# Kernel optimization log

Hardware: AMD Instinct MI355X
Metric: run time of the kernel (lower is better)

Reference implementation:

```python
import jax, jax.numpy as jnp
import numpy as np

SHAPES = ((80, 80), (40, 40), (20, 20), (10, 10))  # (H, W) per level
N_HEADS = 8
N_POINTS = 4
D_MODEL = 512  # double_d_model = 2*256 (densefusion=True)
D_FFN = 1024
B = 2
L = len(SHAPES)
S = sum(h * w for h, w in SHAPES)  # 8500
EPS = 1e-5


def _layernorm(x, g, b):
    m = jnp.mean(x, axis=-1, keepdims=True)
    v = jnp.mean((x - m) ** 2, axis=-1, keepdims=True)
    return (x - m) * jax.lax.rsqrt(v + EPS) * g + b


def _reference_points(shapes):
    # encoder get_reference_points with valid_ratios == 1 -> [S, 2] (x, y) in (0,1)
    refs = []
    for (H, W) in shapes:
        ry = (jnp.arange(H, dtype=jnp.float32) + 0.5) / H
        rx = (jnp.arange(W, dtype=jnp.float32) + 0.5) / W
        gy, gx = jnp.meshgrid(ry, rx, indexing='ij')
        refs.append(jnp.stack([gx.reshape(-1), gy.reshape(-1)], axis=-1))
    return jnp.concatenate(refs, axis=0)


def _sample_level(val, loc, H, W):
    # val: [B, H*W, h, d]; loc: [B, S, h, P, 2] normalized in [0,1]
    b, _, h, d = val.shape
    s, p = loc.shape[1], loc.shape[3]
    x = loc[..., 0] * W - 0.5
    y = loc[..., 1] * H - 0.5
    x0 = jnp.floor(x)
    y0 = jnp.floor(y)
    wx = x - x0
    wy = y - y0
    x0i = x0.astype(jnp.int32)
    y0i = y0.astype(jnp.int32)

    def gather(xi, yi):
        valid = ((xi >= 0) & (xi < W) & (yi >= 0) & (yi < H)).astype(val.dtype)
        idx = jnp.clip(yi, 0, H - 1) * W + jnp.clip(xi, 0, W - 1)  # [B,S,h,P]
        idx2 = jnp.transpose(idx, (0, 1, 3, 2)).reshape(b, s * p, h)  # [B,S*P,h]
        g = jnp.take_along_axis(val, idx2[..., None], axis=1)  # [B,S*P,h,d]
        vmask = jnp.transpose(valid, (0, 1, 3, 2))[..., None]  # [B,S,P,h,1]
        return g.reshape(b, s, p, h, d) * vmask

    v00 = gather(x0i, y0i)
    v01 = gather(x0i + 1, y0i)
    v10 = gather(x0i, y0i + 1)
    v11 = gather(x0i + 1, y0i + 1)
    wxT = jnp.transpose(wx, (0, 1, 3, 2))[..., None]
    wyT = jnp.transpose(wy, (0, 1, 3, 2))[..., None]
    return (v00 * (1 - wxT) * (1 - wyT) + v01 * wxT * (1 - wyT)
            + v10 * (1 - wxT) * wyT + v11 * wxT * wyT)  # [B,S,P,h,d]


def _forward(src, pos, w_off, b_off, w_attn, b_attn, w_val, b_val, w_out, b_out,
             ln1_g, ln1_b, w1, b1, w2, b2, ln2_g, ln2_b, shapes):
    b, s, c = src.shape
    h, p, l = N_HEADS, N_POINTS, len(shapes)
    d = c // h
    q = src + pos
    value = (src @ w_val + b_val).reshape(b, s, h, d)
    offsets = (q @ w_off + b_off).reshape(b, s, h, l, p, 2)
    attn = jax.nn.softmax((q @ w_attn + b_attn).reshape(b, s, h, l * p), axis=-1)
    attn = attn.reshape(b, s, h, l, p)
    ref = _reference_points(shapes)  # [S,2]
    # offset normalizer = (W_l, H_l)
    norm = jnp.array([[W, H] for (H, W) in shapes], dtype=src.dtype)  # [L,2]
    loc = ref[None, :, None, None, None, :] + offsets / norm[None, None, None, :, None, :]
    # split value per level and sample
    starts = np.cumsum([0] + [H * W for (H, W) in shapes])[:-1]
    sampled = []
    for lvl, (H, W) in enumerate(shapes):
        val_l = jax.lax.dynamic_slice_in_dim(value, int(starts[lvl]), H * W, axis=1)
        sampled.append(_sample_level(val_l, loc[:, :, :, lvl], H, W))
    sampled = jnp.stack(sampled)  # [L,B,S,P,h,d]
    out = jnp.einsum('lbqphd,bqhlp->bqhd', sampled, attn).reshape(b, s, c)
    attn_out = out @ w_out + b_out
    x = _layernorm(src + attn_out, ln1_g, ln1_b)
    ffn = jax.nn.relu(x @ w1 + b1) @ w2 + b2
    return _layernorm(x + ffn, ln2_g, ln2_b)


def setup_inputs() -> dict:
    key = jax.random.key(0)
    ks = jax.random.split(key, 20)
    sc = 0.02
    C = D_MODEL
    hLP = N_HEADS * L * N_POINTS
    f32 = jnp.float32
    inp = {
        'src': jax.random.normal(ks[0], (B, S, C), f32),
        'pos': jax.random.normal(ks[1], (B, S, C), f32),
        'w_off': jax.random.normal(ks[2], (C, hLP * 2), f32) * sc,
        'b_off': jax.random.normal(ks[3], (hLP * 2,), f32) * sc,
        'w_attn': jax.random.normal(ks[4], (C, hLP), f32) * sc,
        'b_attn': jax.random.normal(ks[5], (hLP,), f32) * sc,
        'w_val': jax.random.normal(ks[6], (C, C), f32) * sc,
        'b_val': jnp.zeros((C,), f32),
        'w_out': jax.random.normal(ks[7], (C, C), f32) * sc,
        'b_out': jnp.zeros((C,), f32),
        'ln1_g': jnp.ones((C,), f32),
        'ln1_b': jnp.zeros((C,), f32),
        'w1': jax.random.normal(ks[8], (C, D_FFN), f32) * sc,
        'b1': jnp.zeros((D_FFN,), f32),
        'w2': jax.random.normal(ks[9], (D_FFN, C), f32) * sc,
        'b2': jnp.zeros((C,), f32),
        'ln2_g': jnp.ones((C,), f32),
        'ln2_b': jnp.zeros((C,), f32),
        'spatial_shapes': jnp.array(SHAPES, dtype=jnp.int32),
    }
    return inp


def reference(src, pos, w_off, b_off, w_attn, b_attn, w_val, b_val, w_out, b_out,
              ln1_g, ln1_b, w1, b1, w2, b2, ln2_g, ln2_b, spatial_shapes):
    shapes = tuple((int(a), int(b)) for a, b in np.asarray(spatial_shapes))
    return _forward(src, pos, w_off, b_off, w_attn, b_attn, w_val, b_val, w_out, b_out,
                    ln1_g, ln1_b, w1, b1, w2, b2, ln2_g, ln2_b, shapes)
```

## Files before the change

kernel.cpp:

```cpp
#include <hip/hip_runtime.h>


typedef __bf16 bf16_t;
typedef __bf16 bf16x8 __attribute__((ext_vector_type(8)));
typedef __bf16 bf16x4 __attribute__((ext_vector_type(4)));
typedef float  f32x2  __attribute__((ext_vector_type(2)));
typedef float  f32x4  __attribute__((ext_vector_type(4)));
typedef float  f32x16 __attribute__((ext_vector_type(16)));

#define M_ROWS 17000
#define S_LEN  8500

__device__ inline void store_c(float* p, float v)  { *p = v; }
__device__ inline void store_c(bf16_t* p, float v) { *p = (bf16_t)v; }

__device__ inline float4 load4f(const float* p)  { return *(const float4*)p; }
__device__ inline float4 load4f(const bf16_t* p) {
    bf16x4 v = *(const bf16x4*)p;
    return make_float4((float)v[0], (float)v[1], (float)v[2], (float)v[3]);
}

__device__ inline void pk_fma(f32x2& a, f32x2 x, f32x2 y) {
    asm("v_pk_fma_f32 %0, %1, %2, %0" : "+v"(a) : "v"(x), "v"(y));
}

__device__ inline int swz_flat() {
    int o   = blockIdx.x + gridDim.x * blockIdx.y;
    int nwg = gridDim.x * gridDim.y;
    int q = nwg >> 3, r = nwg & 7;
    int xcd = o & 7, s = o >> 3;
    return (xcd < r ? xcd * (q + 1) : r * (q + 1) + (xcd - r) * q) + s;
}

__global__ __launch_bounds__(256)
void prep_kernel(const float* __restrict__ w_val, const float* __restrict__ w_off,
                 const float* __restrict__ w_attn, const float* __restrict__ w_out,
                 const float* __restrict__ w1, const float* __restrict__ w2,
                 const float* __restrict__ b_off, const float* __restrict__ b_attn,
                 bf16_t* __restrict__ wt_val, bf16_t* __restrict__ wt_oa,
                 bf16_t* __restrict__ wt_out, bf16_t* __restrict__ wt_w1,
                 bf16_t* __restrict__ wt_w2, float* __restrict__ bias_oa) {
    int z = blockIdx.z;
    if (z == 6) {
        if (blockIdx.x == 0 && blockIdx.y == 0) {
            for (int i = threadIdx.x; i < 384; i += 256)
                bias_oa[i] = (i < 256) ? b_off[i] : b_attn[i - 256];
        }
        return;
    }
    const float* in; bf16_t* out; int K, N;
    switch (z) {
        case 0: in = w_val;  out = wt_val;                     K = 512;  N = 512;  break;
        case 1: in = w_off;  out = wt_oa;                      K = 512;  N = 256;  break;
        case 2: in = w_attn; out = wt_oa + (size_t)256 * 512;  K = 512;  N = 128;  break;
        case 3: in = w_out;  out = wt_out;                     K = 512;  N = 512;  break;
        case 4: in = w1;     out = wt_w1;                      K = 512;  N = 1024; break;
        default: in = w2;    out = wt_w2;                      K = 1024; N = 512;  break;
    }
    int k0 = blockIdx.x * 32, n0 = blockIdx.y * 32;
    if (k0 >= K || n0 >= N) return;
    __shared__ float s[32][33];
    int tx = threadIdx.x & 31, ty = threadIdx.x >> 5;
    #pragma unroll
    for (int i = 0; i < 4; i++)
        s[ty + 8 * i][tx] = in[(size_t)(k0 + ty + 8 * i) * N + n0 + tx];
    __syncthreads();
    #pragma unroll
    for (int i = 0; i < 4; i++)
        out[(size_t)(n0 + ty + 8 * i) * K + k0 + tx] = (bf16_t)s[tx][ty + 8 * i];
}

__global__ __launch_bounds__(256)
void add_q_kernel(const float* __restrict__ a, const float* __restrict__ b,
                  bf16_t* __restrict__ q, bf16_t* __restrict__ src_bf, int n4) {
    int i = blockIdx.x * 256 + threadIdx.x;
    if (i >= n4) return;
    float4 av = *(const float4*)(a + (size_t)i * 4);
    float4 bv = *(const float4*)(b + (size_t)i * 4);
    bf16x4 sv, ov;
    sv[0] = (bf16_t)av.x; sv[1] = (bf16_t)av.y; sv[2] = (bf16_t)av.z; sv[3] = (bf16_t)av.w;
    ov[0] = (bf16_t)(av.x + bv.x);
    ov[1] = (bf16_t)(av.y + bv.y);
    ov[2] = (bf16_t)(av.z + bv.z);
    ov[3] = (bf16_t)(av.w + bv.w);
    *(bf16x4*)(q      + (size_t)i * 4) = ov;
    *(bf16x4*)(src_bf + (size_t)i * 4) = sv;
}

#define GEMM_CORE(A_PTR, WT_PTR, K_DIM, EPILOGUE)                                  \
    const int tid  = threadIdx.x;                                                  \
    const int wave = tid >> 6;                                                     \
    const int lane = tid & 63;                                                     \
    const int l31  = lane & 31;                                                    \
    const int lh8  = (lane >> 5) * 8;                                              \
    const int wr   = (wave >> 1) * 64;                                             \
    const int wc   = (wave & 1) * 64;                                              \
    const int sr = tid >> 2;                                                       \
    const int sc = (tid & 3) * 8;                                                  \
    const bf16_t* gA0 = A_PTR  + (size_t)min(row0 + sr,      M_ROWS - 1) * (K_DIM) + sc; \
    const bf16_t* gA1 = A_PTR  + (size_t)min(row0 + sr + 64, M_ROWS - 1) * (K_DIM) + sc; \
    const bf16_t* gB0 = WT_PTR + (size_t)(col0 + sr) * (K_DIM) + sc;               \
    const bf16_t* gB1 = WT_PTR + (size_t)(col0 + sr + 64) * (K_DIM) + sc;          \
    f32x16 acc[2][2];                                                              \
    _Pragma("unroll")                                                              \
    for (int i = 0; i < 2; i++)                                                    \
        _Pragma("unroll")                                                          \
        for (int j = 0; j < 2; j++)                                                \
            _Pragma("unroll")                                                      \
            for (int r = 0; r < 16; r++) acc[i][j][r] = 0.f;                       \
    bf16x8 pa0 = *(const bf16x8*)gA0;                                              \
    bf16x8 pa1 = *(const bf16x8*)gA1;                                              \
    bf16x8 pb0 = *(const bf16x8*)gB0;                                              \
    bf16x8 pb1 = *(const bf16x8*)gB1;                                              \
    const int nIter = (K_DIM) >> 5;                                                \
    for (int it = 0; it < nIter; it++) {                                           \
        const int cur = it & 1;                                                    \
        *(bf16x8*)&As[cur][sr][sc]      = pa0;                                     \
        *(bf16x8*)&As[cur][sr + 64][sc] = pa1;                                     \
        *(bf16x8*)&Bs[cur][sr][sc]      = pb0;                                     \
        *(bf16x8*)&Bs[cur][sr + 64][sc] = pb1;                                     \
        __syncthreads();                                                           \
        if (it + 1 < nIter) {                                                      \
            int ko = (it + 1) << 5;                                                \
            pa0 = *(const bf16x8*)(gA0 + ko);                                      \
            pa1 = *(const bf16x8*)(gA1 + ko);                                      \
            pb0 = *(const bf16x8*)(gB0 + ko);                                      \
            pb1 = *(const bf16x8*)(gB1 + ko);                                      \
        }                                                                          \
        _Pragma("unroll")                                                          \
        for (int kh = 0; kh < 2; kh++) {                                           \
            bf16x8 a0 = *(const bf16x8*)&As[cur][wr + l31     ][kh * 16 + lh8];    \
            bf16x8 a1 = *(const bf16x8*)&As[cur][wr + 32 + l31][kh * 16 + lh8];    \
            bf16x8 b0 = *(const bf16x8*)&Bs[cur][wc + l31     ][kh * 16 + lh8];    \
            bf16x8 b1 = *(const bf16x8*)&Bs[cur][wc + 32 + l31][kh * 16 + lh8];    \
            acc[0][0] = __builtin_amdgcn_mfma_f32_32x32x16_bf16(a0, b0, acc[0][0], 0, 0, 0); \
            acc[0][1] = __builtin_amdgcn_mfma_f32_32x32x16_bf16(a0, b1, acc[0][1], 0, 0, 0); \
            acc[1][0] = __builtin_amdgcn_mfma_f32_32x32x16_bf16(a1, b0, acc[1][0], 0, 0, 0); \
            acc[1][1] = __builtin_amdgcn_mfma_f32_32x32x16_bf16(a1, b1, acc[1][1], 0, 0, 0); \
        }                                                                          \
    }                                                                              \
    EPILOGUE

#define GEMM64_CORE(A_PTR, WT_PTR, K_DIM, EPILOGUE)                                \
    const int tid  = threadIdx.x;                                                  \
    const int wave = tid >> 6;                                                     \
    const int lane = tid & 63;                                                     \
    const int l31  = lane & 31;                                                    \
    const int lh8  = (lane >> 5) * 8;                                              \
    const int wr   = wave * 32;                                                    \
    const int sr = tid >> 2;                                                       \
    const int sc = (tid & 3) * 8;                                                  \
    const bf16_t* gA0 = A_PTR  + (size_t)min(row0 + sr,      M_ROWS - 1) * (K_DIM) + sc; \
    const bf16_t* gA1 = A_PTR  + (size_t)min(row0 + sr + 64, M_ROWS - 1) * (K_DIM) + sc; \
    const bf16_t* gB0 = WT_PTR + (size_t)(col0 + sr) * (K_DIM) + sc;               \
    f32x16 acc[2];                                                                 \
    _Pragma("unroll")                                                              \
    for (int j = 0; j < 2; j++)                                                    \
        _Pragma("unroll")                                                          \
        for (int r = 0; r < 16; r++) acc[j][r] = 0.f;                              \
    bf16x8 pa0 = *(const bf16x8*)gA0;                                              \
    bf16x8 pa1 = *(const bf16x8*)gA1;                                              \
    bf16x8 pb0 = *(const bf16x8*)gB0;                                              \
    const int nIter = (K_DIM) >> 5;                                                \
    for (int it = 0; it < nIter; it++) {                                           \
        const int cur = it & 1;                                                    \
        *(bf16x8*)&As[cur][sr][sc]      = pa0;                                     \
        *(bf16x8*)&As[cur][sr + 64][sc] = pa1;                                     \
        *(bf16x8*)&Bs[cur][sr][sc]      = pb0;                                     \
        __syncthreads();                                                           \
        if (it + 1 < nIter) {                                                      \
            int ko = (it + 1) << 5;                                                \
            pa0 = *(const bf16x8*)(gA0 + ko);                                      \
            pa1 = *(const bf16x8*)(gA1 + ko);                                      \
            pb0 = *(const bf16x8*)(gB0 + ko);                                      \
        }                                                                          \
        _Pragma("unroll")                                                          \
        for (int kh = 0; kh < 2; kh++) {                                           \
            bf16x8 a0 = *(const bf16x8*)&As[cur][wr + l31][kh * 16 + lh8];         \
            bf16x8 b0 = *(const bf16x8*)&Bs[cur][l31     ][kh * 16 + lh8];         \
            bf16x8 b1 = *(const bf16x8*)&Bs[cur][32 + l31][kh * 16 + lh8];         \
            acc[0] = __builtin_amdgcn_mfma_f32_32x32x16_bf16(a0, b0, acc[0], 0, 0, 0); \
            acc[1] = __builtin_amdgcn_mfma_f32_32x32x16_bf16(a0, b1, acc[1], 0, 0, 0); \
        }                                                                          \
    }                                                                              \
    EPILOGUE

template<typename OT, bool RELU, int KD>
__global__ __launch_bounds__(256)
void gemm128_kernel(const bf16_t* __restrict__ A, const bf16_t* __restrict__ Wt,
                    const float* __restrict__ bias, OT* __restrict__ Cout, int N) {
    __shared__ bf16_t As[2][128][40];
    __shared__ bf16_t Bs[2][128][40];
    const int wg = swz_flat();
    const int NY = gridDim.y;
    const int row0 = (wg / NY) * 128;
    const int col0 = (wg % NY) * 128;
    GEMM_CORE(A, Wt, KD,
        {
            _Pragma("unroll")
            for (int i = 0; i < 2; i++)
                _Pragma("unroll")
                for (int j = 0; j < 2; j++) {
                    int col = col0 + wc + j * 32 + l31;
                    float bcol = bias[col];
                    _Pragma("unroll")
                    for (int reg = 0; reg < 16; reg++) {
                        int row = row0 + wr + i * 32 + (reg & 3) + 8 * (reg >> 2) + 4 * (lane >> 5);
                        if (row < M_ROWS) {
                            float v = acc[i][j][reg] + bcol;
                            if (RELU) v = fmaxf(v, 0.f);
                            store_c(Cout + (size_t)row * N + col, v);
                        }
                    }
                }
        }
    )
}

template<typename OT, bool RELU, int KD>
__global__ __launch_bounds__(256)
void gemm64_kernel(const bf16_t* __restrict__ A, const bf16_t* __restrict__ Wt,
                   const float* __restrict__ bias, OT* __restrict__ Cout, int N) {
    __shared__ bf16_t As[2][128][40];
    __shared__ bf16_t Bs[2][64][40];
    const int wg = swz_flat();
    const int NY = gridDim.y;
    const int row0 = (wg / NY) * 128;
    const int col0 = (wg % NY) * 64;
    GEMM64_CORE(A, Wt, KD,
        {
            _Pragma("unroll")
            for (int j = 0; j < 2; j++) {
                int col = col0 + j * 32 + l31;
                float bcol = bias[col];
                _Pragma("unroll")
                for (int reg = 0; reg < 16; reg++) {
                    int row = row0 + wr + (reg & 3) + 8 * (reg >> 2) + 4 * (lane >> 5);
                    if (row < M_ROWS) {
                        float v = acc[j][reg] + bcol;
                        if (RELU) v = fmaxf(v, 0.f);
                        store_c(Cout + (size_t)row * N + col, v);
                    }
                }
            }
        }
    )
}

__global__ __launch_bounds__(256)
void gemm_voa_kernel(const bf16_t* __restrict__ src_bf, const bf16_t* __restrict__ q,
                     const bf16_t* __restrict__ wt_val, const bf16_t* __restrict__ wt_oa,
                     const float* __restrict__ b_val, const float* __restrict__ bias_oa,
                     bf16_t* __restrict__ value, float* __restrict__ oa) {
    __shared__ bf16_t As[2][128][40];
    __shared__ bf16_t Bs[2][64][40];
    const int wg = swz_flat();
    const int by = wg % 14;
    const bool isV  = by < 8;
    const int col0  = (isV ? by : by - 8) * 64;
    const int row0  = (wg / 14) * 128;
    const bf16_t* Ap  = isV ? src_bf : q;
    const bf16_t* Wp  = isV ? wt_val : wt_oa;
    const float* bp   = isV ? b_val : bias_oa;
    GEMM64_CORE(Ap, Wp, 512,
        {
            _Pragma("unroll")
            for (int j = 0; j < 2; j++) {
                int col = col0 + j * 32 + l31;
                float bcol = bp[col];
                _Pragma("unroll")
                for (int reg = 0; reg < 16; reg++) {
                    int row = row0 + wr + (reg & 3) + 8 * (reg >> 2) + 4 * (lane >> 5);
                    if (row < M_ROWS) {
                        float v = acc[j][reg] + bcol;
                        if (isV) value[(size_t)row * 512 + col] = (bf16_t)v;
                        else     oa[(size_t)row * 384 + col] = v;
                    }
                }
            }
        }
    )
}

__global__ __launch_bounds__(256)
void sample_kernel(const bf16_t* __restrict__ value, const float* __restrict__ oa,
                   bf16_t* __restrict__ out) {
    __shared__ __align__(16) int sAW[4][2][8][68];
    const int wave = threadIdx.x >> 6;
    const int lane = threadIdx.x & 63;
    const int h    = lane >> 3;
    const int sub  = lane & 7;
    const int bs   = swz_flat() * 4 + wave;
    const int b    = bs / S_LEN;
    const int s    = bs - b * S_LEN;

    float rx, ry;
    if (s < 6400)      { int i = s;        const float inv = 1.f/80.f; ry = ((i/80) + 0.5f)*inv; rx = ((i%80) + 0.5f)*inv; }
    else if (s < 8000) { int i = s - 6400; const float inv = 1.f/40.f; ry = ((i/40) + 0.5f)*inv; rx = ((i%40) + 0.5f)*inv; }
    else if (s < 8400) { int i = s - 8000; const float inv = 1.f/20.f; ry = ((i/20) + 0.5f)*inv; rx = ((i%20) + 0.5f)*inv; }
    else               { int i = s - 8400; const float inv = 1.f/10.f; ry = ((i/10) + 0.5f)*inv; rx = ((i%10) + 0.5f)*inv; }

    const int WH[4]  = {80, 40, 20, 10};
    const int LST[4] = {0, 6400, 8000, 8400};
    const int ll = sub >> 1;
    const int W  = WH[ll];
    const int LS = LST[ll];

    const float* row = oa + (size_t)bs * 384;
    float4 o4 = *(const float4*)(row + h * 32 + sub * 4);
    float2 lg = *(const float2*)(row + 256 + h * 16 + sub * 2);

    float mx = fmaxf(lg.x, lg.y);
    mx = fmaxf(mx, __shfl_xor(mx, 1, 64));
    mx = fmaxf(mx, __shfl_xor(mx, 2, 64));
    mx = fmaxf(mx, __shfl_xor(mx, 4, 64));
    float e0 = __expf(lg.x - mx), e1 = __expf(lg.y - mx);
    float sm = e0 + e1;
    sm += __shfl_xor(sm, 1, 64);
    sm += __shfl_xor(sm, 2, 64);
    sm += __shfl_xor(sm, 4, 64);
    float pinv = 1.f / sm;

    #pragma unroll
    for (int t = 0; t < 2; t++) {
        float ox = t ? o4.z : o4.x;
        float oy = t ? o4.w : o4.y;
        float p  = (t ? e1 : e0) * pinv;
        float x = fmaf(rx, (float)W, ox) - 0.5f;
        float y = fmaf(ry, (float)W, oy) - 0.5f;
        float fx = floorf(x), fy = floorf(y);
        float wx = x - fx, wy = y - fy;
        int ix = (int)fx, iy = (int)fy;
        #pragma unroll
        for (int k2 = 0; k2 < 4; k2++) {
            int cx = ix + (k2 & 1);
            int cy = iy + (k2 >> 1);
            float wgt = p * ((k2 & 1) ? wx : 1.f - wx) * ((k2 >> 1) ? wy : 1.f - wy);
            if (cx < 0 || cx >= W || cy < 0 || cy >= W) wgt = 0.f;
            int xc = min(max(cx, 0), W - 1);
            int yc = min(max(cy, 0), W - 1);
            int c = sub * 8 + t * 4 + k2;
            sAW[wave][0][h][c] = LS + yc * W + xc;
            sAW[wave][1][h][c] = __float_as_int(wgt);
        }
    }
    __syncthreads();

    const bf16_t* vb = value + ((size_t)b * S_LEN) * 512 + h * 64 + sub * 8;
    f32x2 a01 = {0.f, 0.f}, a23 = {0.f, 0.f}, a45 = {0.f, 0.f}, a67 = {0.f, 0.f};

    #define ACC8(V, WW) {                                                          \
        f32x2 ws; ws[0] = (WW); ws[1] = (WW);                                      \
        f32x2 pv;                                                                  \
        pv[0] = __uint_as_float((V).x << 16);                                      \
        pv[1] = __uint_as_float((V).x & 0xffff0000u); pk_fma(a01, pv, ws);         \
        pv[0] = __uint_as_float((V).y << 16);                                      \
        pv[1] = __uint_as_float((V).y & 0xffff0000u); pk_fma(a23, pv, ws);         \
        pv[0] = __uint_as_float((V).z << 16);                                      \
        pv[1] = __uint_as_float((V).z & 0xffff0000u); pk_fma(a45, pv, ws);         \
        pv[0] = __uint_as_float((V).w << 16);                                      \
        pv[1] = __uint_as_float((V).w & 0xffff0000u); pk_fma(a67, pv, ws); }

    #pragma unroll 2
    for (int c8 = 0; c8 < 64; c8 += 8) {
        int4   ia = *(const int4*)  &sAW[wave][0][h][c8];
        int4   ib = *(const int4*)  &sAW[wave][0][h][c8 + 4];
        float4 wa = *(const float4*)&sAW[wave][1][h][c8];
        float4 wb = *(const float4*)&sAW[wave][1][h][c8 + 4];
        uint4 v0 = *(const uint4*)(vb + (size_t)ia.x * 512);
        uint4 v1 = *(const uint4*)(vb + (size_t)ia.y * 512);
        uint4 v2 = *(const uint4*)(vb + (size_t)ia.z * 512);
        uint4 v3 = *(const uint4*)(vb + (size_t)ia.w * 512);
        uint4 v4 = *(const uint4*)(vb + (size_t)ib.x * 512);
        uint4 v5 = *(const uint4*)(vb + (size_t)ib.y * 512);
        uint4 v6 = *(const uint4*)(vb + (size_t)ib.z * 512);
        uint4 v7 = *(const uint4*)(vb + (size_t)ib.w * 512);
        ACC8(v0, wa.x) ACC8(v1, wa.y) ACC8(v2, wa.z) ACC8(v3, wa.w)
        ACC8(v4, wb.x) ACC8(v5, wb.y) ACC8(v6, wb.z) ACC8(v7, wb.w)
    }
    #undef ACC8

    bf16x8 ov;
    ov[0] = (bf16_t)a01[0]; ov[1] = (bf16_t)a01[1];
    ov[2] = (bf16_t)a23[0]; ov[3] = (bf16_t)a23[1];
    ov[4] = (bf16_t)a45[0]; ov[5] = (bf16_t)a45[1];
    ov[6] = (bf16_t)a67[0]; ov[7] = (bf16_t)a67[1];
    *(bf16x8*)(out + (size_t)bs * 512 + h * 64 + sub * 8) = ov;
}

template<typename INA, typename INB, typename OT>
__global__ __launch_bounds__(256)
void ln_kernel(const INA* __restrict__ Xa, const INB* __restrict__ Xb,
               const float* __restrict__ g, const float* __restrict__ be,
               OT* __restrict__ out, int M) {
    int wave = threadIdx.x >> 6;
    int lane = threadIdx.x & 63;
    int row = blockIdx.x * 4 + wave;
    if (row >= M) return;
    size_t base = (size_t)row * 512;
    float v[8];
    float s = 0.f, sq = 0.f;
    #pragma unroll
    for (int p = 0; p < 2; p++) {
        int idx = p * 256 + lane * 4;
        float4 a4 = load4f(Xa + base + idx);
        float4 b4 = load4f(Xb + base + idx);
        float t0 = a4.x + b4.x, t1 = a4.y + b4.y, t2 = a4.z + b4.z, t3 = a4.w + b4.w;
        v[p*4+0] = t0; v[p*4+1] = t1; v[p*4+2] = t2; v[p*4+3] = t3;
        s  += t0 + t1 + t2 + t3;
        sq += t0*t0 + t1*t1 + t2*t2 + t3*t3;
    }
    #pragma unroll
    for (int off = 32; off > 0; off >>= 1) {
        s  += __shfl_xor(s, off, 64);
        sq += __shfl_xor(sq, off, 64);
    }
    float mean = s * (1.f / 512.f);
    float var  = sq * (1.f / 512.f) - mean * mean;
    float rstd = rsqrtf(var + 1e-5f);
    #pragma unroll
    for (int p = 0; p < 2; p++) {
        int idx = p * 256 + lane * 4;
        #pragma unroll
        for (int j = 0; j < 4; j++) {
            int col = idx + j;
            float o = (v[p*4+j] - mean) * rstd * g[col] + be[col];
            store_c(out + base + col, o);
        }
    }
}

extern "C" void kernel_launch(void* const* d_in, const int* in_sizes, int n_in,
                              void* d_out, int out_size, void* d_ws, size_t ws_size,
                              hipStream_t stream) {
    const float* src    = (const float*)d_in[0];
    const float* pos    = (const float*)d_in[1];
    const float* w_off  = (const float*)d_in[2];
    const float* b_off  = (const float*)d_in[3];
    const float* w_attn = (const float*)d_in[4];
    const float* b_attn = (const float*)d_in[5];
    const float* w_val  = (const float*)d_in[6];
    const float* b_val  = (const float*)d_in[7];
    const float* w_out  = (const float*)d_in[8];
    const float* b_out  = (const float*)d_in[9];
    const float* ln1_g  = (const float*)d_in[10];
    const float* ln1_b  = (const float*)d_in[11];
    const float* w1     = (const float*)d_in[12];
    const float* b1     = (const float*)d_in[13];
    const float* w2     = (const float*)d_in[14];
    const float* b2     = (const float*)d_in[15];
    const float* ln2_g  = (const float*)d_in[16];
    const float* ln2_b  = (const float*)d_in[17];

    const int M = M_ROWS;
    char* ws = (char*)d_ws;
    size_t o = 0;
    auto alloc = [&](size_t bytes) { size_t r = o; o += (bytes + 255) & ~(size_t)255; return r; };

    size_t off_q       = alloc((size_t)M * 512 * 2);
    size_t off_srcbf   = alloc((size_t)M * 512 * 2);
    size_t off_value   = alloc((size_t)M * 512 * 2);
    size_t off_sampled = alloc((size_t)M * 512 * 2);
    size_t off_oa      = alloc((size_t)M * 384 * 4);
    size_t off_attnout = alloc((size_t)M * 512 * 2);
    size_t off_x       = alloc((size_t)M * 512 * 2);
    size_t off_wtval   = alloc((size_t)512 * 512 * 2);
    size_t off_wtoa    = alloc((size_t)384 * 512 * 2);
    size_t off_wtout   = alloc((size_t)512 * 512 * 2);
    size_t off_wtw1    = alloc((size_t)1024 * 512 * 2);
    size_t off_wtw2    = alloc((size_t)512 * 1024 * 2);
    size_t off_boa     = alloc((size_t)384 * 4);

    bf16_t* q        = (bf16_t*)(ws + off_q);
    bf16_t* src_bf   = (bf16_t*)(ws + off_srcbf);
    bf16_t* value    = (bf16_t*)(ws + off_value);
    bf16_t* sampled  = (bf16_t*)(ws + off_sampled);
    float*  oa       = (float*)(ws + off_oa);
    bf16_t* attn_out = (bf16_t*)(ws + off_attnout);
    bf16_t* x        = (bf16_t*)(ws + off_x);
    bf16_t* hidden   = (bf16_t*)(ws + off_sampled);
    bf16_t* ffn_out  = (bf16_t*)(ws + off_attnout);
    bf16_t* wt_val   = (bf16_t*)(ws + off_wtval);
    bf16_t* wt_oa    = (bf16_t*)(ws + off_wtoa);
    bf16_t* wt_out   = (bf16_t*)(ws + off_wtout);
    bf16_t* wt_w1    = (bf16_t*)(ws + off_wtw1);
    bf16_t* wt_w2    = (bf16_t*)(ws + off_wtw2);
    float*  bias_oa  = (float*)(ws + off_boa);
    float*  outp     = (float*)d_out;

    prep_kernel<<<dim3(32, 32, 7), 256, 0, stream>>>(
        w_val, w_off, w_attn, w_out, w1, w2, b_off, b_attn,
        wt_val, wt_oa, wt_out, wt_w1, wt_w2, bias_oa);

    add_q_kernel<<<(M * 512 / 4 + 255) / 256, 256, 0, stream>>>(src, pos, q, src_bf, M * 512 / 4);

    const int MT = (M + 127) / 128;

    gemm_voa_kernel<<<dim3(MT, 14), 256, 0, stream>>>(src_bf, q, wt_val, wt_oa, b_val, bias_oa, value, oa);

    sample_kernel<<<M / 4, 256, 0, stream>>>(value, oa, sampled);

    gemm64_kernel<bf16_t, false, 512><<<dim3(MT, 8), 256, 0, stream>>>(sampled, wt_out, b_out, attn_out, 512);

    ln_kernel<float, bf16_t, bf16_t><<<(M + 3) / 4, 256, 0, stream>>>(src, attn_out, ln1_g, ln1_b, x, M);

    gemm128_kernel<bf16_t, true, 512><<<dim3(MT, 8), 256, 0, stream>>>(x, wt_w1, b1, hidden, 1024);
    gemm64_kernel<bf16_t, false, 1024><<<dim3(MT, 8), 256, 0, stream>>>(hidden, wt_w2, b2, ffn_out, 512);

    ln_kernel<bf16_t, bf16_t, float><<<(M + 3) / 4, 256, 0, stream>>>(x, ffn_out, ln2_g, ln2_b, outp, M);
}
```

Baseline: 358.5 us.

## Load GEMM tiles directly into LDS with XOR-swizzled layout

Replaces the register-staged global-to-LDS copies in the GEMM cores with global_load_lds direct transfers into the next double-buffer slot. The LDS tiles lose their padding and use an XOR swizzle on 16-byte chunks to avoid bank conflicts on MFMA operand reads. This saves VGPRs and ds_write instructions and lets the prefetch overlap compute. It relies on the single barrier at the top of each iteration to order the async LDS writes correctly, which carries a race risk if the loads are not waited on.

```diff
diff --git a/kernel.cpp b/kernel.cpp
--- a/kernel.cpp
+++ b/kernel.cpp
@@ -22,6 +22,12 @@
 
 __device__ inline void pk_fma(f32x2& a, f32x2 x, f32x2 y) {
     asm("v_pk_fma_f32 %0, %1, %2, %0" : "+v"(a) : "v"(x), "v"(y));
+}
+
+__device__ __forceinline__ void glds16(const bf16_t* g, bf16_t* l) {
+    __builtin_amdgcn_global_load_lds(
+        (const __attribute__((address_space(1))) void*)g,
+        (__attribute__((address_space(3))) void*)l, 16, 0, 0);
 }
 
 __device__ inline int swz_flat() {
@@ -87,20 +93,25 @@
     *(bf16x4*)(src_bf + (size_t)i * 4) = sv;
 }
 
-#define GEMM_CORE(A_PTR, WT_PTR, K_DIM, EPILOGUE)                                  \
+
+#define GEMM_SETUP                                                                 \
     const int tid  = threadIdx.x;                                                  \
     const int wave = tid >> 6;                                                     \
     const int lane = tid & 63;                                                     \
     const int l31  = lane & 31;                                                    \
-    const int lh8  = (lane >> 5) * 8;                                              \
-    const int wr   = (wave >> 1) * 64;                                             \
-    const int wc   = (wave & 1) * 64;                                              \
-    const int sr = tid >> 2;                                                       \
-    const int sc = (tid & 3) * 8;                                                  \
-    const bf16_t* gA0 = A_PTR  + (size_t)min(row0 + sr,      M_ROWS - 1) * (K_DIM) + sc; \
-    const bf16_t* gA1 = A_PTR  + (size_t)min(row0 + sr + 64, M_ROWS - 1) * (K_DIM) + sc; \
-    const bf16_t* gB0 = WT_PTR + (size_t)(col0 + sr) * (K_DIM) + sc;               \
-    const bf16_t* gB1 = WT_PTR + (size_t)(col0 + sr + 64) * (K_DIM) + sc;          \
+    const int pl   = lane >> 5;                                                    \
+    const int kx   = (l31 >> 1) & 3;                                               \
+    const int st_r = wave * 32 + (lane >> 2);                                      \
+    const int st_c = ((lane & 3) ^ ((lane >> 3) & 3)) * 8;
+
+#define GEMM128_CORE(A_PTR, WT_PTR, K_DIM, EPILOGUE)                               \
+    GEMM_SETUP                                                                     \
+    const int wr = (wave >> 1) * 64;                                               \
+    const int wc = (wave & 1) * 64;                                                \
+    const bf16_t* gsA0 = A_PTR  + (size_t)min(row0 + st_r,      M_ROWS - 1) * (K_DIM) + st_c; \
+    const bf16_t* gsA1 = A_PTR  + (size_t)min(row0 + st_r + 16, M_ROWS - 1) * (K_DIM) + st_c; \
+    const bf16_t* gsB0 = WT_PTR + (size_t)(col0 + st_r) * (K_DIM) + st_c;          \
+    const bf16_t* gsB1 = WT_PTR + (size_t)(col0 + st_r + 16) * (K_DIM) + st_c;     \
     f32x16 acc[2][2];                                                              \
     _Pragma("unroll")                                                              \
     for (int i = 0; i < 2; i++)                                                    \
@@ -108,31 +119,30 @@
         for (int j = 0; j < 2; j++)                                                \
             _Pragma("unroll")                                                      \
             for (int r = 0; r < 16; r++) acc[i][j][r] = 0.f;                       \
-    bf16x8 pa0 = *(const bf16x8*)gA0;                                              \
-    bf16x8 pa1 = *(const bf16x8*)gA1;                                              \
-    bf16x8 pb0 = *(const bf16x8*)gB0;                                              \
-    bf16x8 pb1 = *(const bf16x8*)gB1;                                              \
+    glds16(gsA0, &As[0][wave * 32][0]);                                            \
+    glds16(gsA1, &As[0][wave * 32 + 16][0]);                                       \
+    glds16(gsB0, &Bs[0][wave * 32][0]);                                            \
+    glds16(gsB1, &Bs[0][wave * 32 + 16][0]);                                       \
     const int nIter = (K_DIM) >> 5;                                                \
     for (int it = 0; it < nIter; it++) {                                           \
         const int cur = it & 1;                                                    \
-        *(bf16x8*)&As[cur][sr][sc]      = pa0;                                     \
-        *(bf16x8*)&As[cur][sr + 64][sc] = pa1;                                     \
-        *(bf16x8*)&Bs[cur][sr][sc]      = pb0;                                     \
-        *(bf16x8*)&Bs[cur][sr + 64][sc] = pb1;                                     \
         __syncthreads();                                                           \
         if (it + 1 < nIter) {                                                      \
-            int ko = (it + 1) << 5;                                                \
-            pa0 = *(const bf16x8*)(gA0 + ko);                                      \
-            pa1 = *(const bf16x8*)(gA1 + ko);                                      \
-            pb0 = *(const bf16x8*)(gB0 + ko);                                      \
-            pb1 = *(const bf16x8*)(gB1 + ko);                                      \
+            const int ko = (it + 1) << 5;                                          \
+            glds16(gsA0 + ko, &As[cur ^ 1][wave * 32][0]);                         \
+            glds16(gsA1 + ko, &As[cur ^ 1][wave * 32 + 16][0]);                    \
+            glds16(gsB0 + ko, &Bs[cur ^ 1][wave * 32][0]);                         \
+            glds16(gsB1 + ko, &Bs[cur ^ 1][wave * 32 + 16][0]);                    \
         }                                                                          \
+        const char* Ab = (const char*)&As[cur][0][0];                              \
+        const char* Bb = (const char*)&Bs[cur][0][0];                              \
         _Pragma("unroll")                                                          \
         for (int kh = 0; kh < 2; kh++) {                                           \
-            bf16x8 a0 = *(const bf16x8*)&As[cur][wr + l31     ][kh * 16 + lh8];    \
-            bf16x8 a1 = *(const bf16x8*)&As[cur][wr + 32 + l31][kh * 16 + lh8];    \
-            bf16x8 b0 = *(const bf16x8*)&Bs[cur][wc + l31     ][kh * 16 + lh8];    \
-            bf16x8 b1 = *(const bf16x8*)&Bs[cur][wc + 32 + l31][kh * 16 + lh8];    \
+            const int sA = ((kh * 2 + pl) ^ kx) << 4;                              \
+            bf16x8 a0 = *(const bf16x8*)(Ab + ((wr      + l31) << 6) + sA);        \
+            bf16x8 a1 = *(const bf16x8*)(Ab + ((wr + 32 + l31) << 6) + sA);        \
+            bf16x8 b0 = *(const bf16x8*)(Bb + ((wc      + l31) << 6) + sA);        \
+            bf16x8 b1 = *(const bf16x8*)(Bb + ((wc + 32 + l31) << 6) + sA);        \
             acc[0][0] = __builtin_amdgcn_mfma_f32_32x32x16_bf16(a0, b0, acc[0][0], 0, 0, 0); \
             acc[0][1] = __builtin_amdgcn_mfma_f32_32x32x16_bf16(a0, b1, acc[0][1], 0, 0, 0); \
             acc[1][0] = __builtin_amdgcn_mfma_f32_32x32x16_bf16(a1, b0, acc[1][0], 0, 0, 0); \
@@ -142,43 +152,38 @@
     EPILOGUE
 
 #define GEMM64_CORE(A_PTR, WT_PTR, K_DIM, EPILOGUE)                                \
-    const int tid  = threadIdx.x;                                                  \
-    const int wave = tid >> 6;                                                     \
-    const int lane = tid & 63;                                                     \
-    const int l31  = lane & 31;                                                    \
-    const int lh8  = (lane >> 5) * 8;                                              \
-    const int wr   = wave * 32;                                                    \
-    const int sr = tid >> 2;                                                       \
-    const int sc = (tid & 3) * 8;                                                  \
-    const bf16_t* gA0 = A_PTR  + (size_t)min(row0 + sr,      M_ROWS - 1) * (K_DIM) + sc; \
-    const bf16_t* gA1 = A_PTR  + (size_t)min(row0 + sr + 64, M_ROWS - 1) * (K_DIM) + sc; \
-    const bf16_t* gB0 = WT_PTR + (size_t)(col0 + sr) * (K_DIM) + sc;               \
+    GEMM_SETUP                                                                     \
+    const int wr    = wave * 32;                                                   \
+    const int st_rB = wave * 16 + (lane >> 2);                                     \
+    const bf16_t* gsA0 = A_PTR  + (size_t)min(row0 + st_r,      M_ROWS - 1) * (K_DIM) + st_c; \
+    const bf16_t* gsA1 = A_PTR  + (size_t)min(row0 + st_r + 16, M_ROWS - 1) * (K_DIM) + st_c; \
+    const bf16_t* gsB0 = WT_PTR + (size_t)(col0 + st_rB) * (K_DIM) + st_c;         \
     f32x16 acc[2];                                                                 \
     _Pragma("unroll")                                                              \
     for (int j = 0; j < 2; j++)                                                    \
         _Pragma("unroll")                                                          \
         for (int r = 0; r < 16; r++) acc[j][r] = 0.f;                              \
-    bf16x8 pa0 = *(const bf16x8*)gA0;                                              \
-    bf16x8 pa1 = *(const bf16x8*)gA1;                                              \
-    bf16x8 pb0 = *(const bf16x8*)gB0;                                              \
+    glds16(gsA0, &As[0][wave * 32][0]);                                            \
+    glds16(gsA1, &As[0][wave * 32 + 16][0]);                                       \
+    glds16(gsB0, &Bs[0][wave * 16][0]);                                            \
     const int nIter = (K_DIM) >> 5;                                                \
     for (int it = 0; it < nIter; it++) {                                           \
         const int cur = it & 1;                                                    \
-        *(bf16x8*)&As[cur][sr][sc]      = pa0;                                     \
-        *(bf16x8*)&As[cur][sr + 64][sc] = pa1;                                     \
-        *(bf16x8*)&Bs[cur][sr][sc]      = pb0;                                     \
         __syncthreads();                                                           \
         if (it + 1 < nIter) {                                                      \
-            int ko = (it + 1) << 5;                                                \
-            pa0 = *(const bf16x8*)(gA0 + ko);                                      \
-            pa1 = *(const bf16x8*)(gA1 + ko);                                      \
-            pb0 = *(const bf16x8*)(gB0 + ko);                                      \
+            const int ko = (it + 1) << 5;                                          \
+            glds16(gsA0 + ko, &As[cur ^ 1][wave * 32][0]);                         \
+            glds16(gsA1 + ko, &As[cur ^ 1][wave * 32 + 16][0]);                    \
+            glds16(gsB0 + ko, &Bs[cur ^ 1][wave * 16][0]);                         \
         }                                                                          \
+        const char* Ab = (const char*)&As[cur][0][0];                              \
+        const char* Bb = (const char*)&Bs[cur][0][0];                              \
         _Pragma("unroll")                                                          \
         for (int kh = 0; kh < 2; kh++) {                                           \
-            bf16x8 a0 = *(const bf16x8*)&As[cur][wr + l31][kh * 16 + lh8];         \
-            bf16x8 b0 = *(const bf16x8*)&Bs[cur][l31     ][kh * 16 + lh8];         \
-            bf16x8 b1 = *(const bf16x8*)&Bs[cur][32 + l31][kh * 16 + lh8];         \
+            const int sA = ((kh * 2 + pl) ^ kx) << 4;                              \
+            bf16x8 a0 = *(const bf16x8*)(Ab + ((wr + l31) << 6) + sA);             \
+            bf16x8 b0 = *(const bf16x8*)(Bb + ((     l31) << 6) + sA);             \
+            bf16x8 b1 = *(const bf16x8*)(Bb + ((32 + l31) << 6) + sA);             \
             acc[0] = __builtin_amdgcn_mfma_f32_32x32x16_bf16(a0, b0, acc[0], 0, 0, 0); \
             acc[1] = __builtin_amdgcn_mfma_f32_32x32x16_bf16(a0, b1, acc[1], 0, 0, 0); \
         }                                                                          \
@@ -189,13 +194,13 @@
 __global__ __launch_bounds__(256)
 void gemm128_kernel(const bf16_t* __restrict__ A, const bf16_t* __restrict__ Wt,
                     const float* __restrict__ bias, OT* __restrict__ Cout, int N) {
-    __shared__ bf16_t As[2][128][40];
-    __shared__ bf16_t Bs[2][128][40];
+    __shared__ bf16_t As[2][128][32];
+    __shared__ bf16_t Bs[2][128][32];
     const int wg = swz_flat();
     const int NY = gridDim.y;
     const int row0 = (wg / NY) * 128;
     const int col0 = (wg % NY) * 128;
-    GEMM_CORE(A, Wt, KD,
+    GEMM128_CORE(A, Wt, KD,
         {
             _Pragma("unroll")
             for (int i = 0; i < 2; i++)
@@ -221,8 +226,8 @@
 __global__ __launch_bounds__(256)
 void gemm64_kernel(const bf16_t* __restrict__ A, const bf16_t* __restrict__ Wt,
                    const float* __restrict__ bias, OT* __restrict__ Cout, int N) {
-    __shared__ bf16_t As[2][128][40];
-    __shared__ bf16_t Bs[2][64][40];
+    __shared__ bf16_t As[2][128][32];
+    __shared__ bf16_t Bs[2][64][32];
     const int wg = swz_flat();
     const int NY = gridDim.y;
     const int row0 = (wg / NY) * 128;
@@ -252,8 +257,8 @@
                      const bf16_t* __restrict__ wt_val, const bf16_t* __restrict__ wt_oa,
                      const float* __restrict__ b_val, const float* __restrict__ bias_oa,
                      bf16_t* __restrict__ value, float* __restrict__ oa) {
-    __shared__ bf16_t As[2][128][40];
-    __shared__ bf16_t Bs[2][64][40];
+    __shared__ bf16_t As[2][128][32];
+    __shared__ bf16_t Bs[2][64][32];
     const int wg = swz_flat();
     const int by = wg % 14;
     const bool isV  = by < 8;
```

Measured after the change: 350.5 us (median of 2 runs). 2.2% less time.
